# Optimization experiments

Measured on AMD Instinct MI355X. Metric: run time of the kernel, lower is better.

## Reference

```python
import jax, jax.numpy as jnp
import numpy as np

N, D, F, O = 32768, 32, 128, 128  # nodes, fixed in-degree, in_feats, out_feats


def _lstm_reduce(m, W_ih, W_hh, b_ih, b_hh):
    """Run an LSTM over each node's neighbor mailbox m: [N, T, F] -> final h: [N, H].
    PyTorch gate order: i, f, g, o. W_ih: [4H, F], W_hh: [4H, H]."""
    n, _, _ = m.shape
    H = W_hh.shape[1]
    b = b_ih + b_hh

    def step(carry, x_t):
        h, c = carry
        gates = x_t @ W_ih.T + h @ W_hh.T + b  # [N, 4H]
        i, f, g, o = jnp.split(gates, 4, axis=-1)
        c = jax.nn.sigmoid(f) * c + jax.nn.sigmoid(i) * jnp.tanh(g)
        h = jax.nn.sigmoid(o) * jnp.tanh(c)
        return (h, c), None

    h0 = jnp.zeros((n, H), m.dtype)
    (h_final, _), _ = jax.lax.scan(step, (h0, h0), jnp.swapaxes(m, 0, 1))
    return h_final


def setup_inputs() -> dict:
    key = jax.random.key(0)
    ks = jax.random.split(key, 9)
    stdv_lin = 1.0 / np.sqrt(F)   # linear init: uniform(-1/sqrt(in_feats))
    stdv_lstm = 1.0 / np.sqrt(F)  # torch LSTM init: uniform(-1/sqrt(hidden))
    u = lambda k, shape, s: jax.random.uniform(k, shape, jnp.float32, -s, s)
    return {
        "feat": jax.random.normal(ks[0], (N, F), jnp.float32),
        "neigh_idx": jax.random.randint(ks[1], (N, D), 0, N, jnp.int32),
        "W_ih": u(ks[2], (4 * F, F), stdv_lstm),
        "W_hh": u(ks[3], (4 * F, F), stdv_lstm),
        "b_ih": u(ks[4], (4 * F,), stdv_lstm),
        "b_hh": u(ks[5], (4 * F,), stdv_lstm),
        "W1": u(ks[6], (O, F), stdv_lin),
        "b1": u(ks[6], (O,), stdv_lin),
        "W2": u(ks[7], (O, F), stdv_lin),
        "b2": u(ks[8], (O,), stdv_lin),
    }


def reference(feat, neigh_idx, W_ih, W_hh, b_ih, b_hh, W1, b1, W2, b2):
    # Mailbox gather: each node's D neighbor feature rows -> [N, D, F]
    m = feat[neigh_idx]
    # LSTM reducer -> final hidden state per node
    h = _lstm_reduce(m, W_ih, W_hh, b_ih, b_hh)  # [N, F]
    degs = jnp.asarray(neigh_idx.shape[1], feat.dtype)  # fixed-degree graph
    ah = h / degs
    # feat = linear1(feat) + linear2(ah)
    return feat @ W1.T + b1 + ah @ W2.T + b2
```

## Files before the change

### kernel.cpp

```cpp
#include <hip/hip_runtime.h>
#include <hip/hip_bf16.h>

#define NN 32768
#define DEG 32
#define FF 128
#define OO 128
#define MB 32

typedef __attribute__((ext_vector_type(8))) short bfrag;
typedef __attribute__((ext_vector_type(4))) float f32x4;

#define K1 1.4426950408889634f

__device__ __forceinline__ unsigned short b16(float x) {
    unsigned u = __float_as_uint(x) + 0x8000u;
    return (unsigned short)(u >> 16);
}
__device__ __forceinline__ bfrag pack8(float4 a, float4 b) {
    bfrag r;
    r[0] = (short)b16(a.x); r[1] = (short)b16(a.y); r[2] = (short)b16(a.z); r[3] = (short)b16(a.w);
    r[4] = (short)b16(b.x); r[5] = (short)b16(b.y); r[6] = (short)b16(b.z); r[7] = (short)b16(b.w);
    return r;
}

__device__ __forceinline__ float fsig(float x, float nb) {
    return __builtin_amdgcn_rcpf(1.0f + __builtin_amdgcn_exp2f(fmaf(-K1, x, nb)));
}
__device__ __forceinline__ float ftanh_b(float x, float pb) {
    return fmaf(-2.0f, __builtin_amdgcn_rcpf(1.0f + __builtin_amdgcn_exp2f(fmaf(2.0f * K1, x, pb))), 1.0f);
}
__device__ __forceinline__ float ftanh(float x) {
    return fmaf(-2.0f, __builtin_amdgcn_rcpf(1.0f + __builtin_amdgcn_exp2f(2.0f * K1 * x)), 1.0f);
}

__global__ void prep_weights(const float* __restrict__ wih, const float* __restrict__ whh,
                             const float* __restrict__ b_ih, const float* __restrict__ b_hh,
                             const float* __restrict__ w1, const float* __restrict__ b1,
                             const float* __restrict__ w2, const float* __restrict__ b2,
                             short* __restrict__ wihb, short* __restrict__ whhb,
                             short* __restrict__ w1b, short* __restrict__ w2b,
                             float* __restrict__ biasg, float* __restrict__ biaso)
{
    int i = blockIdx.x * blockDim.x + threadIdx.x;
    if (i < 512 * 128) { wihb[i] = (short)b16(wih[i]); whhb[i] = (short)b16(whh[i]); }
    if (i < 128 * 128) { w1b[i] = (short)b16(w1[i]); w2b[i] = (short)b16(w2[i] * 0.03125f); }
    if (i < 512) biasg[i] = b_ih[i] + b_hh[i];
    if (i < 128) biaso[i] = b1[i] + b2[i];
}

__global__ void prep_feat(const float* __restrict__ f, short* __restrict__ fb) {
    int i = blockIdx.x * blockDim.x + threadIdx.x;
    const float4* p = reinterpret_cast<const float4*>(f) + (size_t)i * 2;
    float4 a = p[0], b = p[1];
    *reinterpret_cast<bfrag*>(fb + (size_t)i * 8) = pack8(a, b);
}

template<bool BF16F>
__device__ __forceinline__ bfrag load_row8(const float* __restrict__ ff, const short* __restrict__ fb,
                                           int node, int cs) {
    if (BF16F) {
        return *reinterpret_cast<const bfrag*>(fb + node * FF + cs * 8);
    } else {
        const float4* p = reinterpret_cast<const float4*>(ff + node * FF + cs * 8);
        return pack8(p[0], p[1]);
    }
}

template<bool BF16F>
__global__ __launch_bounds__(512, 2)
void sage_lstm_kernel(const float* __restrict__ featf, const short* __restrict__ featb,
                      const int* __restrict__ nidx,
                      const short* __restrict__ wihb, const short* __restrict__ whhb,
                      const short* __restrict__ w1b, const short* __restrict__ w2b,
                      const float* __restrict__ biasg, const float* __restrict__ biaso,
                      float* __restrict__ out)
{
    __shared__ short xbuf[2][MB * 128];
    __shared__ short hbuf[2][MB * 128];
    __shared__ int   idx_s[MB * DEG];

    const int tid  = (int)threadIdx.x;
    const int lane = tid & 63;
    const int wave = tid >> 6;
    const int n0   = (int)blockIdx.x * MB;

    const int srow = tid >> 4;
    const int cs   = tid & 15;

    idx_s[tid]       = nidx[n0 * DEG + tid];
    idx_s[512 + tid] = nidx[n0 * DEG + 512 + tid];
    {   bfrag z; for (int j = 0; j < 8; ++j) z[j] = 0;
        reinterpret_cast<bfrag*>(hbuf[0])[tid] = z; }

    const int colw = wave * 16 + (lane & 15);
    bfrag wih[4][4], whh[4][4];
#pragma unroll
    for (int g = 0; g < 4; ++g) {
        const short* pih = wihb + (g * 128 + colw) * FF + (lane >> 4) * 8;
        const short* phh = whhb + (g * 128 + colw) * FF + (lane >> 4) * 8;
#pragma unroll
        for (int kt = 0; kt < 4; ++kt) {
            wih[g][kt] = *reinterpret_cast<const bfrag*>(pih + kt * 32);
            whh[g][kt] = *reinterpret_cast<const bfrag*>(phh + kt * 32);
        }
    }
    const float nbi = -K1 * biasg[colw];
    const float nbf = -K1 * biasg[128 + colw];
    const float pbg = 2.0f * K1 * biasg[256 + colw];
    const float nbo = -K1 * biasg[384 + colw];

    __syncthreads();

    {
        bfrag v = load_row8<BF16F>(featf, featb, idx_s[srow * DEG], cs);
        int sb = (srow * 256 + cs * 16) ^ ((srow & 7) << 4);
        *reinterpret_cast<bfrag*>(reinterpret_cast<char*>(xbuf[0]) + sb) = v;
    }
    __syncthreads();

    const int arow = lane & 15;
    const int asub = (lane >> 4) * 16;
    const int hr0  = (lane >> 4) * 4;
    f32x4 cst[2];
    cst[0] = (f32x4){0.f, 0.f, 0.f, 0.f};
    cst[1] = (f32x4){0.f, 0.f, 0.f, 0.f};

#pragma unroll 2
    for (int t = 0; t < DEG; ++t) {
        const int cur = t & 1;
        char* xcur = reinterpret_cast<char*>(xbuf[cur]);
        char* hcur = reinterpret_cast<char*>(hbuf[cur]);
        char* xnxt = reinterpret_cast<char*>(xbuf[cur ^ 1]);
        char* hnxt = reinterpret_cast<char*>(hbuf[cur ^ 1]);

        bfrag pre;
        if (t < DEG - 1) pre = load_row8<BF16F>(featf, featb, idx_s[srow * DEG + t + 1], cs);

#pragma unroll
        for (int rt = 0; rt < 2; ++rt) {
            const int rowr = rt * 16 + arow;
            const int sw   = (rowr & 7) << 4;
            bfrag xa[4], ha[4];
#pragma unroll
            for (int kt = 0; kt < 4; ++kt) {
                int byte = (rowr * 256 + kt * 64 + asub) ^ sw;
                xa[kt] = *reinterpret_cast<const bfrag*>(xcur + byte);
                ha[kt] = *reinterpret_cast<const bfrag*>(hcur + byte);
            }
            f32x4 gi = {0,0,0,0}, gf = {0,0,0,0}, gg = {0,0,0,0}, go = {0,0,0,0};
#pragma unroll
            for (int kt = 0; kt < 4; ++kt) {
                gi = __builtin_amdgcn_mfma_f32_16x16x32_bf16(xa[kt], wih[0][kt], gi, 0, 0, 0);
                gf = __builtin_amdgcn_mfma_f32_16x16x32_bf16(xa[kt], wih[1][kt], gf, 0, 0, 0);
                gg = __builtin_amdgcn_mfma_f32_16x16x32_bf16(xa[kt], wih[2][kt], gg, 0, 0, 0);
                go = __builtin_amdgcn_mfma_f32_16x16x32_bf16(xa[kt], wih[3][kt], go, 0, 0, 0);
            }
#pragma unroll
            for (int kt = 0; kt < 4; ++kt) {
                gi = __builtin_amdgcn_mfma_f32_16x16x32_bf16(ha[kt], whh[0][kt], gi, 0, 0, 0);
                gf = __builtin_amdgcn_mfma_f32_16x16x32_bf16(ha[kt], whh[1][kt], gf, 0, 0, 0);
                gg = __builtin_amdgcn_mfma_f32_16x16x32_bf16(ha[kt], whh[2][kt], gg, 0, 0, 0);
                go = __builtin_amdgcn_mfma_f32_16x16x32_bf16(ha[kt], whh[3][kt], go, 0, 0, 0);
            }
#pragma unroll
            for (int r = 0; r < 4; ++r) {
                float iv = fsig(gi[r], nbi);
                float fv = fsig(gf[r], nbf);
                float gv = ftanh_b(gg[r], pbg);
                float ov = fsig(go[r], nbo);
                float c  = fmaf(fv, cst[rt][r], iv * gv);
                cst[rt][r] = c;
                float h  = ov * ftanh(c);
                int hrow = rt * 16 + hr0 + r;
                int hb   = (hrow * 256 + colw * 2) ^ ((hrow & 7) << 4);
                *reinterpret_cast<unsigned short*>(hnxt + hb) = b16(h);
            }
        }

        if (t < DEG - 1) {
            int sb = (srow * 256 + cs * 16) ^ ((srow & 7) << 4);
            *reinterpret_cast<bfrag*>(xnxt + sb) = pre;
        }
        __syncthreads();
    }

    {
        bfrag v = load_row8<BF16F>(featf, featb, n0 + srow, cs);
        int sb = (srow * 256 + cs * 16) ^ ((srow & 7) << 4);
        *reinterpret_cast<bfrag*>(reinterpret_cast<char*>(xbuf[0]) + sb) = v;
    }
    __syncthreads();

    bfrag w1f[4], w2f[4];
#pragma unroll
    for (int kt = 0; kt < 4; ++kt) {
        w1f[kt] = *reinterpret_cast<const bfrag*>(w1b + colw * FF + kt * 32 + (lane >> 4) * 8);
        w2f[kt] = *reinterpret_cast<const bfrag*>(w2b + colw * FF + kt * 32 + (lane >> 4) * 8);
    }
    const float bb = biaso[colw];
#pragma unroll
    for (int rt = 0; rt < 2; ++rt) {
        const int rowr = rt * 16 + arow;
        const int sw   = (rowr & 7) << 4;
        bfrag fa[4], hfa[4];
#pragma unroll
        for (int kt = 0; kt < 4; ++kt) {
            int byte = (rowr * 256 + kt * 64 + asub) ^ sw;
            fa[kt]  = *reinterpret_cast<const bfrag*>(reinterpret_cast<char*>(xbuf[0]) + byte);
            hfa[kt] = *reinterpret_cast<const bfrag*>(reinterpret_cast<char*>(hbuf[0]) + byte);
        }
        f32x4 acc = {0.f, 0.f, 0.f, 0.f};
#pragma unroll
        for (int kt = 0; kt < 4; ++kt) {
            acc = __builtin_amdgcn_mfma_f32_16x16x32_bf16(fa[kt],  w1f[kt], acc, 0, 0, 0);
            acc = __builtin_amdgcn_mfma_f32_16x16x32_bf16(hfa[kt], w2f[kt], acc, 0, 0, 0);
        }
#pragma unroll
        for (int r = 0; r < 4; ++r) {
            int orow = n0 + rt * 16 + hr0 + r;
            out[orow * OO + colw] = acc[r] + bb;
        }
    }
}

extern "C" void kernel_launch(void* const* d_in, const int* in_sizes, int n_in,
                              void* d_out, int out_size, void* d_ws, size_t ws_size,
                              hipStream_t stream)
{
    const float* feat = (const float*)d_in[0];
    const int*   nidx = (const int*)d_in[1];
    const float* W_ih = (const float*)d_in[2];
    const float* W_hh = (const float*)d_in[3];
    const float* b_ih = (const float*)d_in[4];
    const float* b_hh = (const float*)d_in[5];
    const float* W1   = (const float*)d_in[6];
    const float* b1   = (const float*)d_in[7];
    const float* W2   = (const float*)d_in[8];
    const float* b2   = (const float*)d_in[9];
    float* out = (float*)d_out;

    char* ws = (char*)d_ws;
    short* wihb  = (short*)(ws);
    short* whhb  = (short*)(ws + 131072);
    short* w1b   = (short*)(ws + 262144);
    short* w2b   = (short*)(ws + 294912);
    float* biasg = (float*)(ws + 327680);
    float* biaso = (float*)(ws + 329728);
    short* featb = (short*)(ws + 330240);

    const size_t need = 330240 + (size_t)NN * FF * 2;
    const bool bf = ws_size >= need;

    prep_weights<<<256, 256, 0, stream>>>(W_ih, W_hh, b_ih, b_hh, W1, b1, W2, b2,
                                          wihb, whhb, w1b, w2b, biasg, biaso);
    if (bf) {
        prep_feat<<<2048, 256, 0, stream>>>(feat, featb);
        sage_lstm_kernel<true><<<NN / MB, 512, 0, stream>>>(feat, featb, nidx, wihb, whhb,
                                                            w1b, w2b, biasg, biaso, out);
    } else {
        sage_lstm_kernel<false><<<NN / MB, 512, 0, stream>>>(feat, featb, nidx, wihb, whhb,
                                                             w1b, w2b, biasg, biaso, out);
    }
}
```

Measured before the change: 315.4 us.

## Software-pipeline LSTM input projection one step ahead of recurrent matmul

The input projection x_t·W_ihᵀ (with the bias folded into the accumulator init) is now computed for step t+1 while step t's recurrent h·W_hhᵀ finishes, and the gather prefetch runs two steps ahead. Only the recurrent MFMA chain stays on the dependency path before the gate activations, so the input MFMAs can overlap with the transcendental math. The bias is now added through the MFMA accumulator rather than fused into the exp2 argument, which costs a few extra ALU ops per gate. Holding eight persistent accumulators adds register pressure that could lower occupancy.

```diff
diff --git a/kernel.cpp b/kernel.cpp
--- a/kernel.cpp
+++ b/kernel.cpp
@@ -23,11 +23,8 @@
     return r;
 }
 
-__device__ __forceinline__ float fsig(float x, float nb) {
-    return __builtin_amdgcn_rcpf(1.0f + __builtin_amdgcn_exp2f(fmaf(-K1, x, nb)));
-}
-__device__ __forceinline__ float ftanh_b(float x, float pb) {
-    return fmaf(-2.0f, __builtin_amdgcn_rcpf(1.0f + __builtin_amdgcn_exp2f(fmaf(2.0f * K1, x, pb))), 1.0f);
+__device__ __forceinline__ float fsig(float x) {
+    return __builtin_amdgcn_rcpf(1.0f + __builtin_amdgcn_exp2f(-K1 * x));
 }
 __device__ __forceinline__ float ftanh(float x) {
     return fmaf(-2.0f, __builtin_amdgcn_rcpf(1.0f + __builtin_amdgcn_exp2f(2.0f * K1 * x)), 1.0f);
@@ -104,10 +101,14 @@
             whh[g][kt] = *reinterpret_cast<const bfrag*>(phh + kt * 32);
         }
     }
-    const float nbi = -K1 * biasg[colw];
-    const float nbf = -K1 * biasg[128 + colw];
-    const float pbg = 2.0f * K1 * biasg[256 + colw];
-    const float nbo = -K1 * biasg[384 + colw];
+    const float bi = biasg[colw];
+    const float bf = biasg[128 + colw];
+    const float bg = biasg[256 + colw];
+    const float bo = biasg[384 + colw];
+    const f32x4 bvi = {bi, bi, bi, bi};
+    const f32x4 bvf = {bf, bf, bf, bf};
+    const f32x4 bvg = {bg, bg, bg, bg};
+    const f32x4 bvo = {bo, bo, bo, bo};
 
     __syncthreads();
 
@@ -121,40 +122,62 @@
     const int arow = lane & 15;
     const int asub = (lane >> 4) * 16;
     const int hr0  = (lane >> 4) * 4;
-    f32x4 cst[2];
-    cst[0] = (f32x4){0.f, 0.f, 0.f, 0.f};
-    cst[1] = (f32x4){0.f, 0.f, 0.f, 0.f};
+    const int swz  = (arow & 7) << 4;
+
+    f32x4 p0i, p0f, p0g, p0o, p1i, p1f, p1g, p1o;
+    {
+        char* x0p = reinterpret_cast<char*>(xbuf[0]);
+        bfrag xa[4];
+#pragma unroll
+        for (int kt = 0; kt < 4; ++kt)
+            xa[kt] = *reinterpret_cast<const bfrag*>(x0p + ((arow * 256 + kt * 64 + asub) ^ swz));
+        p0i = bvi; p0f = bvf; p0g = bvg; p0o = bvo;
+#pragma unroll
+        for (int kt = 0; kt < 4; ++kt) {
+            p0i = __builtin_amdgcn_mfma_f32_16x16x32_bf16(xa[kt], wih[0][kt], p0i, 0, 0, 0);
+            p0f = __builtin_amdgcn_mfma_f32_16x16x32_bf16(xa[kt], wih[1][kt], p0f, 0, 0, 0);
+            p0g = __builtin_amdgcn_mfma_f32_16x16x32_bf16(xa[kt], wih[2][kt], p0g, 0, 0, 0);
+            p0o = __builtin_amdgcn_mfma_f32_16x16x32_bf16(xa[kt], wih[3][kt], p0o, 0, 0, 0);
+        }
+#pragma unroll
+        for (int kt = 0; kt < 4; ++kt)
+            xa[kt] = *reinterpret_cast<const bfrag*>(x0p + (((16 + arow) * 256 + kt * 64 + asub) ^ swz));
+        p1i = bvi; p1f = bvf; p1g = bvg; p1o = bvo;
+#pragma unroll
+        for (int kt = 0; kt < 4; ++kt) {
+            p1i = __builtin_amdgcn_mfma_f32_16x16x32_bf16(xa[kt], wih[0][kt], p1i, 0, 0, 0);
+            p1f = __builtin_amdgcn_mfma_f32_16x16x32_bf16(xa[kt], wih[1][kt], p1f, 0, 0, 0);
+            p1g = __builtin_amdgcn_mfma_f32_16x16x32_bf16(xa[kt], wih[2][kt], p1g, 0, 0, 0);
+            p1o = __builtin_amdgcn_mfma_f32_16x16x32_bf16(xa[kt], wih[3][kt], p1o, 0, 0, 0);
+        }
+    }
+    {
+        bfrag v = load_row8<BF16F>(featf, featb, idx_s[srow * DEG + 1], cs);
+        int sb = (srow * 256 + cs * 16) ^ ((srow & 7) << 4);
+        *reinterpret_cast<bfrag*>(reinterpret_cast<char*>(xbuf[1]) + sb) = v;
+    }
+    __syncthreads();
+
+    f32x4 cs0 = {0.f, 0.f, 0.f, 0.f};
+    f32x4 cs1 = {0.f, 0.f, 0.f, 0.f};
 
 #pragma unroll 2
     for (int t = 0; t < DEG; ++t) {
         const int cur = t & 1;
-        char* xcur = reinterpret_cast<char*>(xbuf[cur]);
         char* hcur = reinterpret_cast<char*>(hbuf[cur]);
-        char* xnxt = reinterpret_cast<char*>(xbuf[cur ^ 1]);
         char* hnxt = reinterpret_cast<char*>(hbuf[cur ^ 1]);
-
-        bfrag pre;
-        if (t < DEG - 1) pre = load_row8<BF16F>(featf, featb, idx_s[srow * DEG + t + 1], cs);
-
-#pragma unroll
-        for (int rt = 0; rt < 2; ++rt) {
-            const int rowr = rt * 16 + arow;
-            const int sw   = (rowr & 7) << 4;
-            bfrag xa[4], ha[4];
-#pragma unroll
-            for (int kt = 0; kt < 4; ++kt) {
-                int byte = (rowr * 256 + kt * 64 + asub) ^ sw;
-                xa[kt] = *reinterpret_cast<const bfrag*>(xcur + byte);
-                ha[kt] = *reinterpret_cast<const bfrag*>(hcur + byte);
-            }
-            f32x4 gi = {0,0,0,0}, gf = {0,0,0,0}, gg = {0,0,0,0}, go = {0,0,0,0};
-#pragma unroll
-            for (int kt = 0; kt < 4; ++kt) {
-                gi = __builtin_amdgcn_mfma_f32_16x16x32_bf16(xa[kt], wih[0][kt], gi, 0, 0, 0);
-                gf = __builtin_amdgcn_mfma_f32_16x16x32_bf16(xa[kt], wih[1][kt], gf, 0, 0, 0);
-                gg = __builtin_amdgcn_mfma_f32_16x16x32_bf16(xa[kt], wih[2][kt], gg, 0, 0, 0);
-                go = __builtin_amdgcn_mfma_f32_16x16x32_bf16(xa[kt], wih[3][kt], go, 0, 0, 0);
-            }
+        char* xrd  = reinterpret_cast<char*>(xbuf[cur ^ 1]);
+        char* xwr  = reinterpret_cast<char*>(xbuf[cur]);
+
+        bfrag pre2;
+        if (t < DEG - 2) pre2 = load_row8<BF16F>(featf, featb, idx_s[srow * DEG + t + 2], cs);
+
+        {
+            bfrag ha[4];
+#pragma unroll
+            for (int kt = 0; kt < 4; ++kt)
+                ha[kt] = *reinterpret_cast<const bfrag*>(hcur + ((arow * 256 + kt * 64 + asub) ^ swz));
+            f32x4 gi = p0i, gf = p0f, gg = p0g, go = p0o;
 #pragma unroll
             for (int kt = 0; kt < 4; ++kt) {
                 gi = __builtin_amdgcn_mfma_f32_16x16x32_bf16(ha[kt], whh[0][kt], gi, 0, 0, 0);
@@ -162,24 +185,79 @@
                 gg = __builtin_amdgcn_mfma_f32_16x16x32_bf16(ha[kt], whh[2][kt], gg, 0, 0, 0);
                 go = __builtin_amdgcn_mfma_f32_16x16x32_bf16(ha[kt], whh[3][kt], go, 0, 0, 0);
             }
+            if (t < DEG - 1) {
+                bfrag xn[4];
+#pragma unroll
+                for (int kt = 0; kt < 4; ++kt)
+                    xn[kt] = *reinterpret_cast<const bfrag*>(xrd + ((arow * 256 + kt * 64 + asub) ^ swz));
+                p0i = bvi; p0f = bvf; p0g = bvg; p0o = bvo;
+#pragma unroll
+                for (int kt = 0; kt < 4; ++kt) {
+                    p0i = __builtin_amdgcn_mfma_f32_16x16x32_bf16(xn[kt], wih[0][kt], p0i, 0, 0, 0);
+                    p0f = __builtin_amdgcn_mfma_f32_16x16x32_bf16(xn[kt], wih[1][kt], p0f, 0, 0, 0);
+                    p0g = __builtin_amdgcn_mfma_f32_16x16x32_bf16(xn[kt], wih[2][kt], p0g, 0, 0, 0);
+                    p0o = __builtin_amdgcn_mfma_f32_16x16x32_bf16(xn[kt], wih[3][kt], p0o, 0, 0, 0);
+                }
+            }
 #pragma unroll
             for (int r = 0; r < 4; ++r) {
-                float iv = fsig(gi[r], nbi);
-                float fv = fsig(gf[r], nbf);
-                float gv = ftanh_b(gg[r], pbg);
-                float ov = fsig(go[r], nbo);
-                float c  = fmaf(fv, cst[rt][r], iv * gv);
-                cst[rt][r] = c;
+                float iv = fsig(gi[r]);
+                float fv = fsig(gf[r]);
+                float gv = ftanh(gg[r]);
+                float ov = fsig(go[r]);
+                float c  = fmaf(fv, cs0[r], iv * gv);
+                cs0[r] = c;
                 float h  = ov * ftanh(c);
-                int hrow = rt * 16 + hr0 + r;
+                int hrow = hr0 + r;
                 int hb   = (hrow * 256 + colw * 2) ^ ((hrow & 7) << 4);
                 *reinterpret_cast<unsigned short*>(hnxt + hb) = b16(h);
             }
         }
-
-        if (t < DEG - 1) {
+        {
+            bfrag ha[4];
+#pragma unroll
+            for (int kt = 0; kt < 4; ++kt)
+                ha[kt] = *reinterpret_cast<const bfrag*>(hcur + (((16 + arow) * 256 + kt * 64 + asub) ^ swz));
+            f32x4 gi = p1i, gf = p1f, gg = p1g, go = p1o;
+#pragma unroll
+            for (int kt = 0; kt < 4; ++kt) {
+                gi = __builtin_amdgcn_mfma_f32_16x16x32_bf16(ha[kt], whh[0][kt], gi, 0, 0, 0);
+                gf = __builtin_amdgcn_mfma_f32_16x16x32_bf16(ha[kt], whh[1][kt], gf, 0, 0, 0);
+                gg = __builtin_amdgcn_mfma_f32_16x16x32_bf16(ha[kt], whh[2][kt], gg, 0, 0, 0);
+                go = __builtin_amdgcn_mfma_f32_16x16x32_bf16(ha[kt], whh[3][kt], go, 0, 0, 0);
+            }
+            if (t < DEG - 1) {
+                bfrag xn[4];
+#pragma unroll
+                for (int kt = 0; kt < 4; ++kt)
+                    xn[kt] = *reinterpret_cast<const bfrag*>(xrd + (((16 + arow) * 256 + kt * 64 + asub) ^ swz));
+                p1i = bvi; p1f = bvf; p1g = bvg; p1o = bvo;
+#pragma unroll
+                for (int kt = 0; kt < 4; ++kt) {
+                    p1i = __builtin_amdgcn_mfma_f32_16x16x32_bf16(xn[kt], wih[0][kt], p1i, 0, 0, 0);
+                    p1f = __builtin_amdgcn_mfma_f32_16x16x32_bf16(xn[kt], wih[1][kt], p1f, 0, 0, 0);
+                    p1g = __builtin_amdgcn_mfma_f32_16x16x32_bf16(xn[kt], wih[2][kt], p1g, 0, 0, 0);
+                    p1o = __builtin_amdgcn_mfma_f32_16x16x32_bf16(xn[kt], wih[3][kt], p1o, 0, 0, 0);
+                }
+            }
+#pragma unroll
+            for (int r = 0; r < 4; ++r) {
+                float iv = fsig(gi[r]);
+                float fv = fsig(gf[r]);
+                float gv = ftanh(gg[r]);
+                float ov = fsig(go[r]);
+                float c  = fmaf(fv, cs1[r], iv * gv);
+                cs1[r] = c;
+                float h  = ov * ftanh(c);
+                int hrow = 16 + hr0 + r;
+                int hb   = (hrow * 256 + colw * 2) ^ ((hrow & 7) << 4);
+                *reinterpret_cast<unsigned short*>(hnxt + hb) = b16(h);
+            }
+        }
+
+        if (t < DEG - 2) {
             int sb = (srow * 256 + cs * 16) ^ ((srow & 7) << 4);
-            *reinterpret_cast<bfrag*>(xnxt + sb) = pre;
+            *reinterpret_cast<bfrag*>(xwr + sb) = pre2;
         }
         __syncthreads();
     }
@@ -201,11 +279,10 @@
 #pragma unroll
     for (int rt = 0; rt < 2; ++rt) {
         const int rowr = rt * 16 + arow;
-        const int sw   = (rowr & 7) << 4;
         bfrag fa[4], hfa[4];
 #pragma unroll
         for (int kt = 0; kt < 4; ++kt) {
-            int byte = (rowr * 256 + kt * 64 + asub) ^ sw;
+            int byte = (rowr * 256 + kt * 64 + asub) ^ swz;
             fa[kt]  = *reinterpret_cast<const bfrag*>(reinterpret_cast<char*>(xbuf[0]) + byte);
             hfa[kt] = *reinterpret_cast<const bfrag*>(reinterpret_cast<char*>(hbuf[0]) + byte);
         }
```

After: 305.9 us. -3.0%, faster.
